# Kernel optimization log

Measured on AMD Instinct MI355X. Metric: run time of the kernel, lower is better.

Reference implementation:

```python
import jax, jax.numpy as jnp
import numpy as np

N_NODES = 100000
N_EDGES = 1600000
D_IN = 128
UNITS = 128


def setup_inputs() -> dict:
    key = jax.random.key(0)
    k1, k2, k3, k4, k5 = jax.random.split(key, 5)
    x = jax.random.normal(k1, (N_NODES, D_IN), dtype=jnp.float32)
    # glorot-uniform-like dense weight
    limit = float(np.sqrt(6.0 / (D_IN + UNITS)))
    w = jax.random.uniform(k2, (D_IN, UNITS), minval=-limit, maxval=limit, dtype=jnp.float32)
    # COO sparse adjacency: A[row, col] = val
    edge_row = jax.random.randint(k3, (N_EDGES,), 0, N_NODES, dtype=jnp.int32)
    edge_col = jax.random.randint(k4, (N_EDGES,), 0, N_NODES, dtype=jnp.int32)
    edge_val = jax.random.uniform(k5, (N_EDGES,), dtype=jnp.float32)
    return {"x": x, "w": w, "edge_row": edge_row, "edge_col": edge_col, "edge_val": edge_val}


def reference(x, w, edge_row, edge_col, edge_val):
    # dropout rate = 0.0 -> identity (module default)
    xw = x @ w                                   # [N, units] dense projection
    # sparse adjacency propagation: out[i] = sum_e val[e] * xw[col[e]] for row[e]==i
    msgs = xw[edge_col] * edge_val[:, None]      # [E, units] irregular gather
    out = jax.ops.segment_sum(msgs, edge_row, num_segments=x.shape[0])
    return jax.nn.relu(out)                      # activation
```

## Files before the change

### kernel.cpp

```cpp
#include <hip/hip_runtime.h>

#define N_NODES 100000
#define N_EDGES 1600000
#define D 128
#define NB 512
#define BCAP 3584
#define BSTRIDE 16
#define CHUNK 4000
#define NSCAT 400
#define NGEMM 1563

typedef __attribute__((ext_vector_type(8))) short  short8;
typedef __attribute__((ext_vector_type(4))) float  floatx4;

__device__ __forceinline__ ushort f2bf(float f) {
    unsigned u = __float_as_uint(f);
    u += 0x7FFF + ((u >> 16) & 1);
    return (ushort)(u >> 16);
}
__device__ __forceinline__ float bf2f(ushort s) {
    return __uint_as_float((unsigned)s << 16);
}
__device__ __forceinline__ int bucket_of(int r)  { return (int)(((unsigned)r << 9) / 100000u); }
__device__ __forceinline__ int row_start(int b)  { return (b * 100000 + 511) >> 9; }

union SMem {
    struct {
        int2  stage[CHUNK];
        int   sA[NB];
        int   sB[NB];
        int   lcur[NB];
        int   gbase[NB];
        short sbuck[CHUNK];
    } sc;
    ushort wt[128 * 128];
};

__global__ __launch_bounds__(256) void gemm_and_scatter(const float* __restrict__ x,
                                                        const float* __restrict__ w,
                                                        ushort* __restrict__ xwb,
                                                        const int* __restrict__ erow,
                                                        const int* __restrict__ ecol,
                                                        const float* __restrict__ eval,
                                                        int* __restrict__ bcnt,
                                                        int2* __restrict__ bkt) {
    __shared__ SMem sm;
    const int t = threadIdx.x;

    if (blockIdx.x < NGEMM) {
        ushort* wt = sm.wt;
        const int wv   = t >> 6;
        const int lane = t & 63;
        const int m    = lane & 15;
        const int q    = lane >> 4;

        {
            const float4* w4 = (const float4*)w;
            for (int i = t; i < 4096; i += 256) {
                const float4 v = w4[i];
                const int k = i >> 5;
                const int n = (i & 31) << 2;
                const int c = k >> 3, kc = k & 7;
#pragma unroll
                for (int d = 0; d < 4; ++d) {
                    const float val = (d == 0) ? v.x : (d == 1) ? v.y : (d == 2) ? v.z : v.w;
                    const int nn = n + d;
                    wt[(nn << 7) | (((c ^ (nn & 15)) & 15) << 3) | kc] = f2bf(val);
                }
            }
        }
        __syncthreads();

        const int rbase = blockIdx.x * 64 + wv * 16;
        if (rbase >= N_NODES) return;

        const float* xrow = x + (size_t)(rbase + m) * D;

        floatx4 acc[8];
#pragma unroll
        for (int tt = 0; tt < 8; ++tt) acc[tt] = (floatx4){0.f, 0.f, 0.f, 0.f};

#pragma unroll
        for (int kk = 0; kk < D; kk += 32) {
            const float4 a0 = *(const float4*)(xrow + kk + q * 8);
            const float4 a1 = *(const float4*)(xrow + kk + q * 8 + 4);
            short8 a;
            a[0] = (short)f2bf(a0.x); a[1] = (short)f2bf(a0.y);
            a[2] = (short)f2bf(a0.z); a[3] = (short)f2bf(a0.w);
            a[4] = (short)f2bf(a1.x); a[5] = (short)f2bf(a1.y);
            a[6] = (short)f2bf(a1.z); a[7] = (short)f2bf(a1.w);

#pragma unroll
            for (int tt = 0; tt < 8; ++tt) {
                const int n  = tt * 16 + m;
                const int cc = (((kk >> 3) + q) ^ m) & 15;
                const short8 b = *(const short8*)&wt[(n << 7) | (cc << 3)];
                acc[tt] = __builtin_amdgcn_mfma_f32_16x16x32_bf16(a, b, acc[tt], 0, 0, 0);
            }
        }

#pragma unroll
        for (int tt = 0; tt < 8; ++tt) {
#pragma unroll
            for (int r = 0; r < 4; ++r) {
                xwb[(size_t)(rbase + q * 4 + r) * D + tt * 16 + m] = f2bf(acc[tt][r]);
            }
        }
    } else {
        const int e0 = (blockIdx.x - NGEMM) * CHUNK;
        int*   sA    = sm.sc.sA;
        int*   sB    = sm.sc.sB;
        int*   lcur  = sm.sc.lcur;
        int*   gbase = sm.sc.gbase;
        short* sbuck = sm.sc.sbuck;
        int2*  stage = sm.sc.stage;

        sA[t] = 0; sA[t + 256] = 0;
        __syncthreads();

        for (int i = t; i < CHUNK; i += 256) {
            atomicAdd(&sA[bucket_of(erow[e0 + i])], 1);
        }
        __syncthreads();

        int cur = 0;
        int* bufs[2] = {sA, sB};
#pragma unroll
        for (int o = 1; o < 512; o <<= 1) {
            const int* src = bufs[cur];
            int*       dst = bufs[cur ^ 1];
            const int i0 = t, i1 = t + 256;
            dst[i0] = src[i0] + ((i0 >= o) ? src[i0 - o] : 0);
            dst[i1] = src[i1] + ((i1 >= o) ? src[i1 - o] : 0);
            cur ^= 1;
            __syncthreads();
        }
        {
            const int* incl = bufs[cur];
            int*       excl = bufs[cur ^ 1];
            excl[t]       = (t == 0) ? 0 : incl[t - 1];
            excl[t + 256] = incl[t + 255];
        }
        __syncthreads();
        int* L = bufs[cur ^ 1];

        for (int b = t; b < NB; b += 256) {
            lcur[b] = L[b];
            const int cnt = ((b == NB - 1) ? CHUNK : L[b + 1]) - L[b];
            gbase[b] = (cnt > 0) ? atomicAdd(&bcnt[b * BSTRIDE], cnt) : 0;
        }
        __syncthreads();

        for (int i = t; i < CHUNK; i += 256) {
            const int   r = erow[e0 + i];
            const int   c = ecol[e0 + i];
            const float v = eval[e0 + i];
            const int   b = bucket_of(r);
            const int  rl = r - row_start(b);
            const int pos = atomicAdd(&lcur[b], 1);
            stage[pos] = make_int2((rl << 17) | c, __float_as_int(v));
            sbuck[pos] = (short)b;
        }
        __syncthreads();

        for (int i = t; i < CHUNK; i += 256) {
            const int b   = sbuck[i];
            const int dst = gbase[b] + (i - L[b]);
            if (dst < BCAP) bkt[(size_t)b * BCAP + dst] = stage[i];
        }
    }
}

__global__ __launch_bounds__(256) void csr_gather(const int* __restrict__ bcnt,
                                                  const int2* __restrict__ bkt,
                                                  const ushort* __restrict__ xwb,
                                                  float* __restrict__ out) {
    __shared__ int2 stage[BCAP];
    __shared__ int2 lcsr[BCAP];
    __shared__ int  sA[256], sB[256], lcur[256];
    const int b = blockIdx.x;
    const int t = threadIdx.x;
    const int n = min(bcnt[b * BSTRIDE], BCAP);
    const int r0    = row_start(b);
    const int nrows = row_start(b + 1) - r0;

    const int2* src = bkt + (size_t)b * BCAP;
    for (int i = t; i < n; i += 256) stage[i] = src[i];
    sA[t] = 0;
    __syncthreads();

    for (int i = t; i < n; i += 256) {
        atomicAdd(&sA[((unsigned)stage[i].x) >> 17], 1);
    }
    __syncthreads();

    int cur = 0;
    int* bufs[2] = {sA, sB};
#pragma unroll
    for (int o = 1; o < 256; o <<= 1) {
        const int* s = bufs[cur];
        int*       d = bufs[cur ^ 1];
        d[t] = s[t] + ((t >= o) ? s[t - o] : 0);
        cur ^= 1;
        __syncthreads();
    }
    lcur[t] = (t == 0) ? 0 : bufs[cur][t - 1];
    __syncthreads();

    for (int i = t; i < n; i += 256) {
        const int2 e = stage[i];
        const int rl = ((unsigned)e.x) >> 17;
        const int pos = atomicAdd(&lcur[rl], 1);
        lcsr[pos] = make_int2(e.x & 0x1FFFF, e.y);
    }
    __syncthreads();

    const int wv = t >> 6;
    const int l  = t & 63;
    const int q  = l >> 4;
    const int lc = (l & 15) << 3;

    for (int ln = wv; ln < nrows; ln += 4) {
        const int start = (ln == 0) ? 0 : lcur[ln - 1];
        const int end   = lcur[ln];

        float acc0[8] = {0, 0, 0, 0, 0, 0, 0, 0};
        float acc1[8] = {0, 0, 0, 0, 0, 0, 0, 0};
        float acc2[8] = {0, 0, 0, 0, 0, 0, 0, 0};
        float acc3[8] = {0, 0, 0, 0, 0, 0, 0, 0};

        for (int j0 = start + q; j0 < end; j0 += 16) {
            const int jb = j0 + 4, jc = j0 + 8, jd = j0 + 12;
            const int2 cva = lcsr[j0];
            const int2 cvb = lcsr[min(jb, end - 1)];
            const int2 cvc = lcsr[min(jc, end - 1)];
            const int2 cvd = lcsr[min(jd, end - 1)];
            const short8 ma = *(const short8*)&xwb[(size_t)cva.x * D + lc];
            const short8 mb = *(const short8*)&xwb[(size_t)cvb.x * D + lc];
            const short8 mc = *(const short8*)&xwb[(size_t)cvc.x * D + lc];
            const short8 md = *(const short8*)&xwb[(size_t)cvd.x * D + lc];
            const float va = __int_as_float(cva.y);
            const float vb = (jb < end) ? __int_as_float(cvb.y) : 0.f;
            const float vc = (jc < end) ? __int_as_float(cvc.y) : 0.f;
            const float vd = (jd < end) ? __int_as_float(cvd.y) : 0.f;
#pragma unroll
            for (int i = 0; i < 8; ++i) {
                acc0[i] += va * bf2f((ushort)ma[i]);
                acc1[i] += vb * bf2f((ushort)mb[i]);
                acc2[i] += vc * bf2f((ushort)mc[i]);
                acc3[i] += vd * bf2f((ushort)md[i]);
            }
        }

#pragma unroll
        for (int i = 0; i < 8; ++i) {
            float s = (acc0[i] + acc1[i]) + (acc2[i] + acc3[i]);
            s += __shfl_down(s, 32);
            s += __shfl_down(s, 16);
            acc0[i] = fmaxf(s, 0.f);
        }

        if (q == 0) {
            float* o = out + (size_t)(r0 + ln) * D + lc;
            *(float4*)(o + 0) = make_float4(acc0[0], acc0[1], acc0[2], acc0[3]);
            *(float4*)(o + 4) = make_float4(acc0[4], acc0[5], acc0[6], acc0[7]);
        }
    }
}

extern "C" void kernel_launch(void* const* d_in, const int* in_sizes, int n_in,
                              void* d_out, int out_size, void* d_ws, size_t ws_size,
                              hipStream_t stream) {
    const float* x    = (const float*)d_in[0];
    const float* w    = (const float*)d_in[1];
    const int*   erow = (const int*)d_in[2];
    const int*   ecol = (const int*)d_in[3];
    const float* eval = (const float*)d_in[4];
    float*       out  = (float*)d_out;

    char*   ws_base = (char*)d_ws;
    ushort* xwb  = (ushort*)ws_base;
    int*    bcnt = (int*)(ws_base + 25600000);
    int2*   bkt  = (int2*)(ws_base + 25632768);

    (void)hipMemsetAsync(bcnt, 0, 32768, stream);

    gemm_and_scatter<<<NGEMM + NSCAT, 256, 0, stream>>>(x, w, xwb, erow, ecol, eval, bcnt, bkt);
    csr_gather<<<NB, 256, 0, stream>>>(bcnt, bkt, xwb, out);
}
```

Baseline: 230.3 us.

## Split each bucket's gather across two blocks to raise occupancy

The CSR gather kernel now launches two blocks per bucket, each owning half the bucket's rows. Each block filters edges straight from global memory instead of staging the whole bucket in LDS, so it needs much less shared memory. It also declares a minimum of 4 blocks per CU. This is meant to increase parallelism and occupancy for the latency-bound gather. In exchange, each block rereads the full bucket twice from global/L2 memory, and a tighter per-half capacity could drop edges if a half overflows.

```diff
diff --git a/kernel.cpp b/kernel.cpp
--- a/kernel.cpp
+++ b/kernel.cpp
@@ -9,6 +9,7 @@
 #define CHUNK 4000
 #define NSCAT 400
 #define NGEMM 1563
+#define HCAP 1792
 
 typedef __attribute__((ext_vector_type(8))) short  short8;
 typedef __attribute__((ext_vector_type(4))) float  floatx4;
@@ -171,26 +172,31 @@
     }
 }
 
-__global__ __launch_bounds__(256) void csr_gather(const int* __restrict__ bcnt,
-                                                  const int2* __restrict__ bkt,
-                                                  const ushort* __restrict__ xwb,
-                                                  float* __restrict__ out) {
-    __shared__ int2 stage[BCAP];
-    __shared__ int2 lcsr[BCAP];
+__global__ __launch_bounds__(256, 4) void csr_gather(const int* __restrict__ bcnt,
+                                                     const int2* __restrict__ bkt,
+                                                     const ushort* __restrict__ xwb,
+                                                     float* __restrict__ out) {
+    __shared__ int2 lcsr[HCAP];
     __shared__ int  sA[256], sB[256], lcur[256];
-    const int b = blockIdx.x;
-    const int t = threadIdx.x;
-    const int n = min(bcnt[b * BSTRIDE], BCAP);
+    const int bg = blockIdx.x;
+    const int b  = bg >> 1;
+    const int h  = bg & 1;
+    const int t  = threadIdx.x;
+    const int n  = min(bcnt[b * BSTRIDE], BCAP);
     const int r0    = row_start(b);
     const int nrows = row_start(b + 1) - r0;
+    const int mid   = (nrows + 1) >> 1;
+    const int lo    = h ? mid : 0;
+    const int hi    = h ? nrows : mid;
+    const int nloc  = hi - lo;
 
     const int2* src = bkt + (size_t)b * BCAP;
-    for (int i = t; i < n; i += 256) stage[i] = src[i];
     sA[t] = 0;
     __syncthreads();
 
     for (int i = t; i < n; i += 256) {
-        atomicAdd(&sA[((unsigned)stage[i].x) >> 17], 1);
+        const int rl = (int)(((unsigned)src[i].x) >> 17);
+        if (rl >= lo && rl < hi) atomicAdd(&sA[rl - lo], 1);
     }
     __syncthreads();
 
@@ -208,10 +214,12 @@
     __syncthreads();
 
     for (int i = t; i < n; i += 256) {
-        const int2 e = stage[i];
-        const int rl = ((unsigned)e.x) >> 17;
-        const int pos = atomicAdd(&lcur[rl], 1);
-        lcsr[pos] = make_int2(e.x & 0x1FFFF, e.y);
+        const int2 e = src[i];
+        const int rl = (int)(((unsigned)e.x) >> 17);
+        if (rl >= lo && rl < hi) {
+            const int pos = atomicAdd(&lcur[rl - lo], 1);
+            if (pos < HCAP) lcsr[pos] = make_int2(e.x & 0x1FFFF, e.y);
+        }
     }
     __syncthreads();
 
@@ -220,9 +228,11 @@
     const int q  = l >> 4;
     const int lc = (l & 15) << 3;
 
-    for (int ln = wv; ln < nrows; ln += 4) {
-        const int start = (ln == 0) ? 0 : lcur[ln - 1];
-        const int end   = lcur[ln];
+    for (int ln = wv; ln < nloc; ln += 4) {
+        int start = (ln == 0) ? 0 : lcur[ln - 1];
+        int end   = lcur[ln];
+        start = min(start, HCAP);
+        end   = min(end, HCAP);
 
         float acc0[8] = {0, 0, 0, 0, 0, 0, 0, 0};
         float acc1[8] = {0, 0, 0, 0, 0, 0, 0, 0};
@@ -261,7 +271,7 @@
         }
 
         if (q == 0) {
-            float* o = out + (size_t)(r0 + ln) * D + lc;
+            float* o = out + (size_t)(r0 + lo + ln) * D + lc;
             *(float4*)(o + 0) = make_float4(acc0[0], acc0[1], acc0[2], acc0[3]);
             *(float4*)(o + 4) = make_float4(acc0[4], acc0[5], acc0[6], acc0[7]);
         }
@@ -286,5 +296,5 @@
     (void)hipMemsetAsync(bcnt, 0, 32768, stream);
 
     gemm_and_scatter<<<NGEMM + NSCAT, 256, 0, stream>>>(x, w, xwb, erow, ecol, eval, bcnt, bkt);
-    csr_gather<<<NB, 256, 0, stream>>>(bcnt, bkt, xwb, out);
-}
+    csr_gather<<<NB * 2, 256, 0, stream>>>(bcnt, bkt, xwb, out);
+}
```

Result: no change. 229.7 us (-0.3%).
